# Optimization experiments

Hardware: AMD Instinct MI355X
Metric: run time of the kernel (lower is better)

The kernel has to match this reference:

```python
import jax, jax.numpy as jnp
import numpy as np

B, T, IN, E, D, O = 32, 256, 64, 128, 128, 32


def _lstm_scan(x_tbi, Wih, Whh, b, h0, c0):
    # x_tbi: [T,B,in]; returns hidden states [T,B,H]; PyTorch gate order i,f,g,o
    def step(carry, xt):
        h, c = carry
        z = xt @ Wih.T + h @ Whh.T + b
        i, f, g, o = jnp.split(z, 4, axis=-1)
        c = jax.nn.sigmoid(f) * c + jax.nn.sigmoid(i) * jnp.tanh(g)
        h = jax.nn.sigmoid(o) * jnp.tanh(c)
        return (h, c), h
    _, hs = jax.lax.scan(step, (h0, c0), x_tbi)
    return hs


def setup_inputs() -> dict:
    key = jax.random.key(0)
    ks = jax.random.split(key, 20)
    def u(k, shape, fan):
        s = 1.0 / np.sqrt(fan)
        return jax.random.uniform(k, shape, jnp.float32, -s, s)
    x = jax.random.normal(ks[0], (B, T, IN), jnp.float32)
    lengths = jnp.sort(jax.random.randint(ks[1], (B,), T // 2, T + 1))[::-1]
    lengths = lengths.at[0].set(T)  # pad_packed max length == T
    return {
        "x": x,
        "input_lengths": lengths,
        "dec_h0": jax.random.normal(ks[2], (B, D), jnp.float32),
        "dec_c0": jax.random.normal(ks[3], (B, D), jnp.float32),
        "Wih_f": u(ks[4], (4 * E, IN), E), "Whh_f": u(ks[5], (4 * E, E), E), "b_f": u(ks[6], (4 * E,), E),
        "Wih_b": u(ks[7], (4 * E, IN), E), "Whh_b": u(ks[8], (4 * E, E), E), "b_b": u(ks[9], (4 * E,), E),
        "Wa": u(ks[10], (D, D + 2 * E), D + 2 * E), "ba": u(ks[11], (D,), D + 2 * E),
        "v": jax.random.uniform(ks[12], (D,), jnp.float32, 0.0, 1.0),
        "Wih_d": u(ks[13], (4 * D, 2 * E + O), D), "Whh_d": u(ks[14], (4 * D, D), D), "b_d": u(ks[15], (4 * D,), D),
        "Wl": u(ks[16], (O, 2 * E + D), 2 * E + D), "bl": u(ks[17], (O,), 2 * E + D),
    }


def _forward(x, input_lengths, dec_h0, dec_c0, Wih_f, Whh_f, b_f, Wih_b, Whh_b, b_b,
             Wa, ba, v, Wih_d, Whh_d, b_d, Wl, bl):
    mask = jnp.arange(T)[None, :] < input_lengths[:, None]  # [B,T] valid positions
    z0 = jnp.zeros((B, E), x.dtype)
    # --- bidirectional encoder (packed-sequence semantics) ---
    hf = _lstm_scan(x.transpose(1, 0, 2), Wih_f, Whh_f, b_f, z0, z0).transpose(1, 0, 2)  # [B,T,E]
    # backward dir: reverse each valid span, scan, reverse back
    rev_idx = jnp.where(mask, input_lengths[:, None] - 1 - jnp.arange(T)[None, :], 0)  # [B,T]
    xr = jnp.take_along_axis(x, rev_idx[:, :, None], axis=1)
    hb_r = _lstm_scan(xr.transpose(1, 0, 2), Wih_b, Whh_b, b_b, z0, z0).transpose(1, 0, 2)
    hb = jnp.take_along_axis(hb_r, rev_idx[:, :, None], axis=1)
    enc = jnp.concatenate([hf, hb], -1) * mask[:, :, None]  # [B,T,2E], zeros past length
    # --- decoder with additive attention ---
    Wa_h, Wa_e = Wa[:, :D], Wa[:, D:]
    enc_proj = enc @ Wa_e.T + ba  # [B,T,D], constant across decoder steps
    def dec_step(carry, _):
        hidden, y = carry
        e = jnp.tanh(enc_proj + (hidden @ Wa_h.T)[:, None, :])  # [B,T,D]
        s = jnp.where(mask, e @ v, -jnp.inf)                     # length-masked scores
        a = jax.nn.softmax(s, axis=1)
        ctx = jnp.einsum('bt,bte->be', a, enc)                   # [B,2E]
        di = jnp.concatenate([y, ctx], -1)                       # [B,O+2E]
        # NOTE: original resets the decoder LSTM to (dec_h0, dec_c0) every step
        z = di @ Wih_d.T + dec_h0 @ Whh_d.T + b_d
        i, f, g, o = jnp.split(z, 4, axis=-1)
        c = jax.nn.sigmoid(f) * dec_c0 + jax.nn.sigmoid(i) * jnp.tanh(g)
        h = jax.nn.sigmoid(o) * jnp.tanh(c)
        y_new = jnp.concatenate([h, ctx], -1) @ Wl.T + bl        # [B,O]
        return (h, y_new), y_new
    y0 = jnp.zeros((B, O), x.dtype)
    _, ys = jax.lax.scan(dec_step, (dec_h0, y0), None, length=T)  # [T,B,O]
    out = ys.transpose(1, 0, 2).reshape(B, T * O)
    # original prepends a zeros[B,O] block then slices [:, 1:]
    out = jnp.concatenate([jnp.zeros((B, O), x.dtype), out], axis=1)
    return out[:, 1:]


def reference(x, input_lengths, dec_h0, dec_c0, Wih_f, Whh_f, b_f, Wih_b, Whh_b, b_b,
              Wa, ba, v, Wih_d, Whh_d, b_d, Wl, bl):
    return _forward(x, input_lengths, dec_h0, dec_c0, Wih_f, Whh_f, b_f, Wih_b, Whh_b, b_b,
                    Wa, ba, v, Wih_d, Whh_d, b_d, Wl, bl)
```

## Files before the change

kernel.cpp:

```cpp
#include <hip/hip_runtime.h>

#define BB 32
#define TT 256
#define INP 64
#define EE 128
#define DD 128
#define OO 32

#define OFF_XWF    0u
#define OFF_ENCWH  0u
#define OFF_XWB    4194304u
#define OFF_EPT    4194304u
#define OFF_ENCWLH 5242880u
#define OFF_HF     8388608u
#define OFF_HBR    9437184u
#define OFF_ZC     10485760u
#define OFF_WHHTF  10502144u
#define OFF_WHHTB  10567680u
#define OFF_WIHTF  10633216u
#define OFF_WIHTB  10665984u
#define OFF_WHHDT  10698752u
#define OFF_WCAT   10764288u
#define OFF_WLHT   10936320u
#define OFF_WAHH   10940416u
#define OFF_WYH    10948608u

typedef _Float16 h2_t __attribute__((ext_vector_type(2)));

__device__ __forceinline__ float fexp2(float x){ return __builtin_amdgcn_exp2f(x); }
__device__ __forceinline__ float frcp(float x){ return __builtin_amdgcn_rcpf(x); }
__device__ __forceinline__ float fsig(float x){ return frcp(1.0f + fexp2(-1.4426950408889634f * x)); }
__device__ __forceinline__ float ftanh_(float x){ return 1.0f - 2.0f * frcp(1.0f + fexp2(2.8853900817779268f * x)); }
__device__ __forceinline__ float packh2(float a, float b){
  h2_t t; t.x = (_Float16)a; t.y = (_Float16)b; return __builtin_bit_cast(float, t);
}
__device__ __forceinline__ h2_t ash2(float f){ return __builtin_bit_cast(h2_t, f); }
__device__ __forceinline__ float fdot2_(float a, float b, float c){
  return __builtin_amdgcn_fdot2(ash2(a), ash2(b), c, false);
}

#define C2F 2.8853900817779268f
#define L2E 1.4426950408889634f

__global__ void pack_kernel(const float* __restrict__ Whh_f, const float* __restrict__ Whh_b,
                            const float* __restrict__ Wih_f, const float* __restrict__ Wih_b,
                            const float* __restrict__ Whh_d, const float* __restrict__ Wa,
                            const float* __restrict__ Wih_d, const float* __restrict__ Wl,
                            float* __restrict__ ws){
  unsigned e = blockIdx.x * 256u + threadIdx.x;
  if (e < 65536u){ unsigned j=e>>7, k=e&127u; ws[OFF_WHHTF + (k>>2)*2048u + j*4u + (k&3u)] = Whh_f[e]; return; }
  e -= 65536u;
  if (e < 65536u){ unsigned j=e>>7, k=e&127u; ws[OFF_WHHTB + (k>>2)*2048u + j*4u + (k&3u)] = Whh_b[e]; return; }
  e -= 65536u;
  if (e < 32768u){ unsigned j=e>>6, i=e&63u; ws[OFF_WIHTF + (i>>2)*2048u + j*4u + (i&3u)] = Wih_f[e]; return; }
  e -= 32768u;
  if (e < 32768u){ unsigned j=e>>6, i=e&63u; ws[OFF_WIHTB + (i>>2)*2048u + j*4u + (i&3u)] = Wih_b[e]; return; }
  e -= 32768u;
  if (e < 65536u){ unsigned j=e>>7, k=e&127u; ws[OFF_WHHDT + (k>>2)*2048u + j*4u + (k&3u)] = Whh_d[e]; return; }
  e -= 65536u;
  if (e < 172032u){
    unsigned j = e >> 8, k = e & 255u;
    float val;
    if (j < 128u)      val = Wa[j*384u + 128u + k];
    else if (j < 640u) val = Wih_d[(j-128u)*288u + 32u + k];
    else               val = Wl[(j-640u)*384u + 128u + k];
    ws[OFF_WCAT + (k>>2)*2688u + j*4u + (k&3u)] = val; return;
  }
  e -= 172032u;
  if (e < 4096u){ unsigned k=e>>5, m=e&31u; ws[OFF_WLHT + (k>>2)*128u + m*4u + (k&3u)] = Wl[m*384u + k]; return; }
  e -= 4096u;
  if (e < 8192u){
    unsigned d = e >> 6, k2 = e & 63u;
    ws[OFF_WAHH + e] = packh2(Wa[d*384u + 2u*k2], Wa[d*384u + 2u*k2 + 1u]); return;
  }
  e -= 8192u;
  if (e < 8192u){
    unsigned m2 = e >> 9, j = e & 511u;
    ws[OFF_WYH + e] = packh2(Wih_d[j*288u + 2u*m2], Wih_d[j*288u + 2u*m2 + 1u]); return;
  }
}

__global__ __launch_bounds__(512) void zc_kernel(const float* __restrict__ dec_h0,
                                                 const float* __restrict__ b_d,
                                                 float* __restrict__ ws){
  __shared__ __align__(16) float h0[128];
  int b = blockIdx.x, j = threadIdx.x;
  if (j < 128) h0[j] = dec_h0[b*128 + j];
  __syncthreads();
  const float* WT = ws + OFF_WHHDT;
  float4 a4 = make_float4(0.f,0.f,0.f,0.f);
  #pragma unroll
  for (int k4 = 0; k4 < 32; k4++){
    float4 wv = *(const float4*)(WT + k4*2048 + j*4);
    float4 hv = *(const float4*)(h0 + k4*4);
    a4.x += wv.x*hv.x; a4.y += wv.y*hv.y; a4.z += wv.z*hv.z; a4.w += wv.w*hv.w;
  }
  ws[OFF_ZC + b*512 + j] = b_d[j] + (a4.x + a4.y) + (a4.z + a4.w);
}

__global__ __launch_bounds__(512) void xw_kernel(const float* __restrict__ x,
                                                 const int* __restrict__ lengths,
                                                 const float* __restrict__ b_f,
                                                 const float* __restrict__ b_b,
                                                 float* __restrict__ ws){
  int bx = blockIdx.x;
  int dir = bx >> 9, b = (bx >> 4) & 31, tile = bx & 15;
  int t0 = tile * 16;
  int len = lengths[b];
  __shared__ __align__(16) float xrow[16][64];
  const float* WT   = ws + (dir ? OFF_WIHTB : OFF_WIHTF);
  const float* bias = dir ? b_b : b_f;
  float* out = ws + (dir ? OFF_XWB : OFF_XWF) + (unsigned)b * TT * 512;
  int tid = threadIdx.x;
  for (int idx = tid; idx < 1024; idx += 512){
    int r = idx >> 6, i = idx & 63;
    int s = t0 + r;
    int src = dir ? ((s < len) ? (len - 1 - s) : 0) : s;
    xrow[r][i] = x[((unsigned)b * TT + src) * 64 + i];
  }
  __syncthreads();
  int j = tid;
  float bj = bias[j];
  float acc[16];
  #pragma unroll
  for (int r = 0; r < 16; r++) acc[r] = bj;
  #pragma unroll 4
  for (int i4 = 0; i4 < 16; i4++){
    float4 wv = *(const float4*)(WT + i4*2048 + j*4);
    #pragma unroll
    for (int r = 0; r < 16; r++){
      float4 xv = *(const float4*)(&xrow[r][i4*4]);
      acc[r] += wv.x*xv.x + wv.y*xv.y + wv.z*xv.z + wv.w*xv.w;
    }
  }
  #pragma unroll
  for (int r = 0; r < 16; r++) out[(t0 + r)*512 + j] = acc[r];
}

__global__ __launch_bounds__(512, 2) void lstm_kernel(const int* __restrict__ lengths,
                                                      float* __restrict__ ws){
  int bx = blockIdx.x;
  int b = bx & 31, dir = bx >> 5;
  int len = lengths[b];
  if (len < 1) len = 1; if (len > TT) len = TT;
  const float* xW = ws + (dir ? OFF_XWB : OFF_XWF) + (unsigned)b * TT * 512;
  const float* WT = ws + (dir ? OFF_WHHTB : OFF_WHHTF);
  float* hout = ws + (dir ? OFF_HBR : OFF_HF) + (unsigned)b * TT * 128;
  __shared__ __align__(16) float hsh[128];
  __shared__ __align__(16) float csh[128];
  __shared__ __align__(16) float zsh[512];
  int j = threadIdx.x;
  float w[128];
  #pragma unroll
  for (int k4 = 0; k4 < 32; k4++){
    float4 wv = *(const float4*)(WT + k4*2048 + j*4);
    w[k4*4+0] = wv.x; w[k4*4+1] = wv.y; w[k4*4+2] = wv.z; w[k4*4+3] = wv.w;
  }
  if (j < 128){ hsh[j] = 0.f; csh[j] = 0.f; }
  for (int t = 0; t < len; t++){
    __syncthreads();
    float4 a4 = make_float4(xW[t*512 + j], 0.f, 0.f, 0.f);
    #pragma unroll
    for (int k4 = 0; k4 < 32; k4++){
      float4 hv = *(const float4*)(hsh + k4*4);
      a4.x += w[k4*4+0]*hv.x; a4.y += w[k4*4+1]*hv.y;
      a4.z += w[k4*4+2]*hv.z; a4.w += w[k4*4+3]*hv.w;
    }
    zsh[j] = (a4.x + a4.y) + (a4.z + a4.w);
    __syncthreads();
    if (j < 128){
      float zi = zsh[j], zf = zsh[128+j], zg = zsh[256+j], zo = zsh[384+j];
      float c = fsig(zf)*csh[j] + fsig(zi)*ftanh_(zg);
      float h = fsig(zo)*ftanh_(c);
      csh[j] = c; hsh[j] = h;
      hout[t*128 + j] = h;
    }
  }
}

__global__ __launch_bounds__(192) void proj_kernel(const int* __restrict__ lengths,
                                                   const float* __restrict__ ba,
                                                   float* __restrict__ ws){
  int bx = blockIdx.x;
  int b = bx >> 4, tile = bx & 15;
  int len = lengths[b];
  if (len < 1) len = 1; if (len > TT) len = TT;
  int t0 = tile * 16;
  __shared__ __align__(16) float enc[16][256];
  int tid = threadIdx.x;
  const float* hf  = ws + OFF_HF  + (unsigned)b * TT * 128;
  const float* hbr = ws + OFF_HBR + (unsigned)b * TT * 128;
  for (int idx = tid; idx < 4096; idx += 192){
    int r = idx >> 8, k = idx & 255;
    int t = t0 + r;
    float vv = 0.f;
    if (t < len) vv = (k < 128) ? hf[t*128 + k] : hbr[(len-1-t)*128 + (k-128)];
    enc[r][k] = vv;
  }
  __syncthreads();
  if (tid >= 168) return;
  int j0 = tid * 4;
  float acc[16][4];
  #pragma unroll
  for (int r = 0; r < 16; r++){ acc[r][0]=0.f; acc[r][1]=0.f; acc[r][2]=0.f; acc[r][3]=0.f; }
  const float* WC = ws + OFF_WCAT;
  for (int k4 = 0; k4 < 64; k4++){
    float4 w0 = *(const float4*)(WC + k4*2688 + (j0+0)*4);
    float4 w1 = *(const float4*)(WC + k4*2688 + (j0+1)*4);
    float4 w2 = *(const float4*)(WC + k4*2688 + (j0+2)*4);
    float4 w3 = *(const float4*)(WC + k4*2688 + (j0+3)*4);
    #pragma unroll
    for (int r = 0; r < 16; r++){
      float4 ev = *(const float4*)(&enc[r][k4*4]);
      acc[r][0] += w0.x*ev.x + w0.y*ev.y + w0.z*ev.z + w0.w*ev.w;
      acc[r][1] += w1.x*ev.x + w1.y*ev.y + w1.z*ev.z + w1.w*ev.w;
      acc[r][2] += w2.x*ev.x + w2.y*ev.y + w2.z*ev.z + w2.w*ev.w;
      acc[r][3] += w3.x*ev.x + w3.y*ev.y + w3.z*ev.z + w3.w*ev.w;
    }
  }
  float* epo  = ws + OFF_EPT    + (unsigned)b * TT * 128;
  float* eWh  = ws + OFF_ENCWH  + (unsigned)b * 128 * 512;
  float* eWlh = ws + OFF_ENCWLH + (unsigned)b * 128 * 32;
  #pragma unroll
  for (int c = 0; c < 4; c++){
    int j = j0 + c;
    if (j < 128){
      float bj = ba[j];
      for (int r = 0; r < 16; r++) epo[(t0 + r)*128 + j] = (acc[r][c] + bj) * C2F;
    } else if (j < 640){
      for (int r2 = 0; r2 < 8; r2++)
        eWh[(tile*8 + r2)*512 + (j - 128)] = packh2(acc[2*r2][c], acc[2*r2+1][c]);
    } else {
      for (int r2 = 0; r2 < 8; r2++)
        eWlh[(tile*8 + r2)*32 + (j - 640)] = packh2(acc[2*r2][c], acc[2*r2+1][c]);
    }
  }
}

__global__ __launch_bounds__(512, 2) void decoder_kernel(const int* __restrict__ lengths,
                                                         const float* __restrict__ dec_h0,
                                                         const float* __restrict__ dec_c0,
                                                         const float* __restrict__ v,
                                                         const float* __restrict__ bl,
                                                         float* __restrict__ ws,
                                                         float* __restrict__ out){
  __shared__ __align__(16) float ep_lds[32768];
  __shared__ __align__(16) float red512[512];
  __shared__ __align__(16) float zsh[512];
  __shared__ __align__(16) float vqsh[256];
  __shared__ __align__(16) float hsh[128];
  __shared__ __align__(16) float c0sh[128];
  __shared__ __align__(16) float a_h2[128];
  __shared__ __align__(16) float h_h2[64];
  __shared__ __align__(16) float ylds[32];
  __shared__ __align__(16) float y_h2[16];
  __shared__ float redbuf[2], redbuf2[2], vsumsh;

  int b = blockIdx.x;
  int len = lengths[b];
  if (len < 1) len = 1; if (len > TT) len = TT;
  int tid = threadIdx.x;

  const float* EPT  = ws + OFF_EPT    + (unsigned)b * 32768;
  const float* EWH  = ws + OFF_ENCWH  + (unsigned)b * 65536;
  const float* EWLH = ws + OFF_ENCWLH + (unsigned)b * 4096;
  const float* WLHT = ws + OFF_WLHT;
  float* outp = out + (unsigned)b * 8223;

  float wreg[128];
  #pragma unroll
  for (int r = 0; r < 128; r++) wreg[r] = EWH[r*512 + tid];
  int d_ = tid & 127, p_ = tid >> 7;
  float wah[16];
  #pragma unroll
  for (int i = 0; i < 16; i++) wah[i] = ws[OFF_WAHH + d_*64 + p_*16 + i];
  float wy[16];
  #pragma unroll
  for (int i = 0; i < 16; i++) wy[i] = ws[OFF_WYH + i*512 + tid];
  float zc_r = ws[OFF_ZC + b*512 + tid];

  for (int c = 0; c < 64; c++){
    int idx = c*512 + tid;
    int t = idx >> 7, dd = idx & 127;
    ep_lds[t*128 + ((dd + 4*t) & 127)] = EPT[idx];
  }
  if (tid < 128){
    hsh[tid]  = dec_h0[b*128 + tid];
    c0sh[tid] = dec_c0[b*128 + tid];
    vqsh[2*tid+1] = v[tid];
  }
  if (tid < 64) h_h2[tid] = packh2(dec_h0[b*128 + 2*tid], dec_h0[b*128 + 2*tid + 1]);
  if (tid < 32) ylds[tid] = 0.f;
  if (tid < 16) y_h2[tid] = 0.f;
  if (tid < 31) outp[tid] = 0.f;
  if (tid == 0){ float s = 0.f; for (int k = 0; k < 128; k++) s += v[k]; vsumsh = s; }

  for (int t = 0; t < TT; t++){
    __syncthreads();
    if (tid < 16) y_h2[tid] = packh2(ylds[2*tid], ylds[2*tid+1]);
    {
      float qa = 0.f, qb = 0.f;
      #pragma unroll
      for (int i = 0; i < 16; i += 2){
        qa = fdot2_(h_h2[p_*16 + i],     wah[i],     qa);
        qb = fdot2_(h_h2[p_*16 + i + 1], wah[i + 1], qb);
      }
      red512[tid] = qa + qb;
    }
    __syncthreads();
    if (tid < 128)
      vqsh[2*tid] = (red512[tid] + red512[128+tid] + red512[256+tid] + red512[384+tid]) * C2F;
    __syncthreads();
    {
      int tt = tid & 255, half = tid >> 8;
      float4 P4 = make_float4(0.f,0.f,0.f,0.f);
      if (tt < len){
        const float* epr = ep_lds + tt*128;
        int rot = 4*tt;
        #pragma unroll 4
        for (int g = 0; g < 16; g++){
          int d0 = (half*16 + g)*4;
          float4 e4 = *(const float4*)(epr + ((d0 + rot) & 127));
          float4 vq0 = *(const float4*)(vqsh + 2*d0);
          float4 vq1 = *(const float4*)(vqsh + 2*d0 + 4);
          P4.x = fmaf(vq0.y, frcp(1.f + fexp2(e4.x + vq0.x)), P4.x);
          P4.y = fmaf(vq0.w, frcp(1.f + fexp2(e4.y + vq0.z)), P4.y);
          P4.z = fmaf(vq1.y, frcp(1.f + fexp2(e4.z + vq1.x)), P4.z);
          P4.w = fmaf(vq1.w, frcp(1.f + fexp2(e4.w + vq1.z)), P4.w);
        }
      }
      red512[tid] = (P4.x + P4.y) + (P4.z + P4.w);
    }
    __syncthreads();
    float s0 = -1e30f, s1 = -1e30f, e0 = 0.f, e1 = 0.f;
    if (tid < 128){
      int ta = 2*tid;
      if (ta < len)     s0 = vsumsh - 2.f*(red512[ta]   + red512[256+ta]);
      if (ta + 1 < len) s1 = vsumsh - 2.f*(red512[ta+1] + red512[256+ta+1]);
    }
    {
      float mm = fmaxf(s0, s1);
      #pragma unroll
      for (int off = 32; off; off >>= 1) mm = fmaxf(mm, __shfl_xor(mm, off));
      if (tid < 128 && (tid & 63) == 0) redbuf[tid>>6] = mm;
    }
    __syncthreads();
    if (tid < 128){
      float gm = fmaxf(redbuf[0], redbuf[1]);
      if (2*tid < len)     e0 = fexp2((s0 - gm) * L2E);
      if (2*tid + 1 < len) e1 = fexp2((s1 - gm) * L2E);
    }
    {
      float ss = e0 + e1;
      #pragma unroll
      for (int off = 32; off; off >>= 1) ss += __shfl_xor(ss, off);
      if (tid < 128 && (tid & 63) == 0) redbuf2[tid>>6] = ss;
    }
    __syncthreads();
    if (tid < 128){
      float rl = frcp(redbuf2[0] + redbuf2[1]);
      a_h2[tid] = packh2(e0 * rl, e1 * rl);
    }
    __syncthreads();
    {
      float za = 0.f, zb = 0.f, zc2 = 0.f, zd = 0.f;
      #pragma unroll
      for (int r4 = 0; r4 < 32; r4++){
        za  = fdot2_(a_h2[4*r4+0], wreg[4*r4+0], za);
        zb  = fdot2_(a_h2[4*r4+1], wreg[4*r4+1], zb);
        zc2 = fdot2_(a_h2[4*r4+2], wreg[4*r4+2], zc2);
        zd  = fdot2_(a_h2[4*r4+3], wreg[4*r4+3], zd);
      }
      #pragma unroll
      for (int i4 = 0; i4 < 4; i4++){
        za  = fdot2_(y_h2[4*i4+0], wy[4*i4+0], za);
        zb  = fdot2_(y_h2[4*i4+1], wy[4*i4+1], zb);
        zc2 = fdot2_(y_h2[4*i4+2], wy[4*i4+2], zc2);
        zd  = fdot2_(y_h2[4*i4+3], wy[4*i4+3], zd);
      }
      zsh[tid] = zc_r + ((za + zb) + (zc2 + zd));
    }
    __syncthreads();
    if (tid < 128){
      float zi = zsh[tid], zf = zsh[128+tid], zg = zsh[256+tid], zo = zsh[384+tid];
      float c = fsig(zf)*c0sh[tid] + fsig(zi)*ftanh_(zg);
      hsh[tid] = fsig(zo)*ftanh_(c);
    }
    __syncthreads();
    if (tid >= 256 && tid < 320){
      int i = tid - 256;
      h_h2[i] = packh2(hsh[2*i], hsh[2*i+1]);
    }
    if (tid < 256){
      int m = tid & 31, p = tid >> 5;
      float acc = 0.f;
      #pragma unroll
      for (int ri = 0; ri < 16; ri++){
        int r = p + ri*8;
        acc = fdot2_(a_h2[r], EWLH[r*32 + m], acc);
      }
      #pragma unroll
      for (int k4 = p; k4 < 32; k4 += 8){
        float4 hv = *(const float4*)(hsh + k4*4);
        float4 wv = *(const float4*)(WLHT + k4*128 + m*4);
        acc += hv.x*wv.x + hv.y*wv.y + hv.z*wv.z + hv.w*wv.w;
      }
      red512[tid] = acc;
    }
    __syncthreads();
    if (tid < 32){
      float y = bl[tid];
      #pragma unroll
      for (int p2 = 0; p2 < 8; p2++) y += red512[p2*32 + tid];
      ylds[tid] = y;
      outp[31 + t*32 + tid] = y;
    }
  }
}

extern "C" void kernel_launch(void* const* d_in, const int* in_sizes, int n_in,
                              void* d_out, int out_size, void* d_ws, size_t ws_size,
                              hipStream_t stream){
  const float* x       = (const float*)d_in[0];
  const int*   lengths = (const int*)  d_in[1];
  const float* dec_h0  = (const float*)d_in[2];
  const float* dec_c0  = (const float*)d_in[3];
  const float* Wih_f   = (const float*)d_in[4];
  const float* Whh_f   = (const float*)d_in[5];
  const float* b_f     = (const float*)d_in[6];
  const float* Wih_b   = (const float*)d_in[7];
  const float* Whh_b   = (const float*)d_in[8];
  const float* b_b     = (const float*)d_in[9];
  const float* Wa      = (const float*)d_in[10];
  const float* ba      = (const float*)d_in[11];
  const float* v       = (const float*)d_in[12];
  const float* Wih_d   = (const float*)d_in[13];
  const float* Whh_d   = (const float*)d_in[14];
  const float* b_d     = (const float*)d_in[15];
  const float* Wl      = (const float*)d_in[16];
  const float* bl      = (const float*)d_in[17];
  float* ws  = (float*)d_ws;
  float* out = (float*)d_out;

  pack_kernel<<<1776, 256, 0, stream>>>(Whh_f, Whh_b, Wih_f, Wih_b, Whh_d, Wa, Wih_d, Wl, ws);
  zc_kernel<<<32, 512, 0, stream>>>(dec_h0, b_d, ws);
  xw_kernel<<<1024, 512, 0, stream>>>(x, lengths, b_f, b_b, ws);
  lstm_kernel<<<64, 512, 0, stream>>>(lengths, ws);
  proj_kernel<<<512, 192, 0, stream>>>(lengths, ba, ws);
  decoder_kernel<<<32, 512, 0, stream>>>(lengths, dec_h0, dec_c0, v, bl, ws, out);
}
```

Before: 1.988 ms.

## Widen decoder to 1024 threads and cut per-step barriers

Doubles the decoder block to 1024 threads and splits the attention-context GEMV and score computation across more threads with fewer registers each. The output-projection reduction and the next step's query projection move into the tail of the previous step, so the loop needs fewer barriers. The softmax max pass is dropped in favor of clamped exponentials. The sigmoid sum shares one reciprocal between pairs of terms. Wl and bias are staged in LDS. Dropping max-subtraction relies on bounded scores and risks overflow or precision loss. The 4-blocks-per-CU launch bound may also force register spills.

```diff
diff --git a/kernel.cpp b/kernel.cpp
--- a/kernel.cpp
+++ b/kernel.cpp
@@ -237,24 +237,25 @@
   }
 }
 
-__global__ __launch_bounds__(512, 2) void decoder_kernel(const int* __restrict__ lengths,
-                                                         const float* __restrict__ dec_h0,
-                                                         const float* __restrict__ dec_c0,
-                                                         const float* __restrict__ v,
-                                                         const float* __restrict__ bl,
-                                                         float* __restrict__ ws,
-                                                         float* __restrict__ out){
+__global__ __launch_bounds__(1024, 4) void decoder_kernel(const int* __restrict__ lengths,
+                                                          const float* __restrict__ dec_h0,
+                                                          const float* __restrict__ dec_c0,
+                                                          const float* __restrict__ v,
+                                                          const float* __restrict__ bl,
+                                                          float* __restrict__ ws,
+                                                          float* __restrict__ out){
   __shared__ __align__(16) float ep_lds[32768];
-  __shared__ __align__(16) float red512[512];
-  __shared__ __align__(16) float zsh[512];
+  __shared__ __align__(16) float wlh_lds[4096];
+  __shared__ __align__(16) float red[1024];
   __shared__ __align__(16) float vqsh[256];
+  __shared__ __align__(16) float zcsh[512];
   __shared__ __align__(16) float hsh[128];
   __shared__ __align__(16) float c0sh[128];
-  __shared__ __align__(16) float a_h2[128];
-  __shared__ __align__(16) float h_h2[64];
-  __shared__ __align__(16) float ylds[32];
+  __shared__ __align__(16) _Float16 h_h16[128];
+  __shared__ __align__(16) _Float16 a_h16[256];
   __shared__ __align__(16) float y_h2[16];
-  __shared__ float redbuf[2], redbuf2[2], vsumsh;
+  __shared__ __align__(16) float blsh[32];
+  __shared__ float swave[4], vsumsh;
 
   int b = blockIdx.x;
   int len = lengths[b];
@@ -264,157 +265,175 @@
   const float* EPT  = ws + OFF_EPT    + (unsigned)b * 32768;
   const float* EWH  = ws + OFF_ENCWH  + (unsigned)b * 65536;
   const float* EWLH = ws + OFF_ENCWLH + (unsigned)b * 4096;
-  const float* WLHT = ws + OFF_WLHT;
   float* outp = out + (unsigned)b * 8223;
 
-  float wreg[128];
-  #pragma unroll
-  for (int r = 0; r < 128; r++) wreg[r] = EWH[r*512 + tid];
-  int d_ = tid & 127, p_ = tid >> 7;
+  int j_ = tid & 511, dh_ = tid >> 9;
+  int d_ = tid & 127, p_ = (tid >> 7) & 3;
+  float wreg[64];
+  #pragma unroll
+  for (int r = 0; r < 64; r++) wreg[r] = EWH[(dh_*64 + r)*512 + j_];
   float wah[16];
   #pragma unroll
   for (int i = 0; i < 16; i++) wah[i] = ws[OFF_WAHH + d_*64 + p_*16 + i];
-  float wy[16];
-  #pragma unroll
-  for (int i = 0; i < 16; i++) wy[i] = ws[OFF_WYH + i*512 + tid];
-  float zc_r = ws[OFF_ZC + b*512 + tid];
-
-  for (int c = 0; c < 64; c++){
-    int idx = c*512 + tid;
+  float wy[8];
+  #pragma unroll
+  for (int i = 0; i < 8; i++) wy[i] = ws[OFF_WYH + (dh_*8 + i)*512 + j_];
+
+  for (int c = 0; c < 32; c++){
+    int idx = c*1024 + tid;
     int t = idx >> 7, dd = idx & 127;
     ep_lds[t*128 + ((dd + 4*t) & 127)] = EPT[idx];
   }
+  for (int c = 0; c < 4; c++) wlh_lds[c*1024 + tid] = ws[OFF_WLHT + c*1024 + tid];
+  if (tid < 512) zcsh[tid] = ws[OFF_ZC + b*512 + tid];
   if (tid < 128){
-    hsh[tid]  = dec_h0[b*128 + tid];
+    float h0v = dec_h0[b*128 + tid];
+    hsh[tid] = h0v; h_h16[tid] = (_Float16)h0v;
     c0sh[tid] = dec_c0[b*128 + tid];
     vqsh[2*tid+1] = v[tid];
   }
-  if (tid < 64) h_h2[tid] = packh2(dec_h0[b*128 + 2*tid], dec_h0[b*128 + 2*tid + 1]);
-  if (tid < 32) ylds[tid] = 0.f;
   if (tid < 16) y_h2[tid] = 0.f;
+  if (tid < 32) blsh[tid] = bl[tid];
   if (tid < 31) outp[tid] = 0.f;
   if (tid == 0){ float s = 0.f; for (int k = 0; k < 128; k++) s += v[k]; vsumsh = s; }
+  __syncthreads();
+  if (tid >= 256 && tid < 768){
+    const float* hp = (const float*)h_h16;
+    float qa = 0.f, qb = 0.f;
+    #pragma unroll
+    for (int i = 0; i < 16; i += 2){
+      qa = fdot2_(hp[p_*16 + i],     wah[i],     qa);
+      qb = fdot2_(hp[p_*16 + i + 1], wah[i + 1], qb);
+    }
+    red[256 + p_*128 + d_] = qa + qb;
+  }
+  __syncthreads();
 
   for (int t = 0; t < TT; t++){
-    __syncthreads();
-    if (tid < 16) y_h2[tid] = packh2(ylds[2*tid], ylds[2*tid+1]);
+    if (tid < 128){
+      float q = red[256+tid] + red[384+tid] + red[512+tid] + red[640+tid];
+      vqsh[2*tid] = q * C2F;
+    } else if (tid < 144 && t > 0){
+      int m0 = 2*(tid - 128);
+      float ya = blsh[m0], yb = blsh[m0+1];
+      #pragma unroll
+      for (int p2 = 0; p2 < 8; p2++){ ya += red[p2*32 + m0]; yb += red[p2*32 + m0 + 1]; }
+      y_h2[tid - 128] = packh2(ya, yb);
+      outp[31 + (t-1)*32 + m0]     = ya;
+      outp[31 + (t-1)*32 + m0 + 1] = yb;
+    }
+    __syncthreads();
     {
-      float qa = 0.f, qb = 0.f;
-      #pragma unroll
-      for (int i = 0; i < 16; i += 2){
-        qa = fdot2_(h_h2[p_*16 + i],     wah[i],     qa);
-        qb = fdot2_(h_h2[p_*16 + i + 1], wah[i + 1], qb);
-      }
-      red512[tid] = qa + qb;
-    }
-    __syncthreads();
-    if (tid < 128)
-      vqsh[2*tid] = (red512[tid] + red512[128+tid] + red512[256+tid] + red512[384+tid]) * C2F;
-    __syncthreads();
-    {
-      int tt = tid & 255, half = tid >> 8;
-      float4 P4 = make_float4(0.f,0.f,0.f,0.f);
-      if (tt < len){
-        const float* epr = ep_lds + tt*128;
-        int rot = 4*tt;
-        #pragma unroll 4
-        for (int g = 0; g < 16; g++){
-          int d0 = (half*16 + g)*4;
-          float4 e4 = *(const float4*)(epr + ((d0 + rot) & 127));
+      int t_ = tid & 255, q4 = tid >> 8;
+      float P = 0.f;
+      if (t_ < len){
+        const float* epr = ep_lds + t_*128;
+        int rot = 4*t_;
+        float pa = 0.f, pb = 0.f, pc = 0.f, pd = 0.f;
+        #pragma unroll
+        for (int g = 0; g < 8; g++){
+          int d0 = q4*32 + g*4;
+          float4 e4  = *(const float4*)(epr + ((d0 + rot) & 127));
           float4 vq0 = *(const float4*)(vqsh + 2*d0);
           float4 vq1 = *(const float4*)(vqsh + 2*d0 + 4);
-          P4.x = fmaf(vq0.y, frcp(1.f + fexp2(e4.x + vq0.x)), P4.x);
-          P4.y = fmaf(vq0.w, frcp(1.f + fexp2(e4.y + vq0.z)), P4.y);
-          P4.z = fmaf(vq1.y, frcp(1.f + fexp2(e4.z + vq1.x)), P4.z);
-          P4.w = fmaf(vq1.w, frcp(1.f + fexp2(e4.w + vq1.z)), P4.w);
+          float E0 = fexp2(fminf(e4.x + vq0.x, 60.f));
+          float E1 = fexp2(fminf(e4.y + vq0.z, 60.f));
+          float E2 = fexp2(fminf(e4.z + vq1.x, 60.f));
+          float E3 = fexp2(fminf(e4.w + vq1.z, 60.f));
+          float D0 = 1.f + E0, D1 = 1.f + E1, D2 = 1.f + E2, D3 = 1.f + E3;
+          float r01 = frcp(D0*D1), r23 = frcp(D2*D3);
+          pa = fmaf(vq0.y*D1, r01, pa);
+          pb = fmaf(vq0.w*D0, r01, pb);
+          pc = fmaf(vq1.y*D3, r23, pc);
+          pd = fmaf(vq1.w*D2, r23, pd);
         }
-      }
-      red512[tid] = (P4.x + P4.y) + (P4.z + P4.w);
-    }
-    __syncthreads();
-    float s0 = -1e30f, s1 = -1e30f, e0 = 0.f, e1 = 0.f;
+        P = (pa + pb) + (pc + pd);
+      }
+      red[tid] = P;
+    }
+    __syncthreads();
+    float e_t = 0.f;
+    if (tid < 256){
+      float P = red[tid] + red[256+tid] + red[512+tid] + red[768+tid];
+      if (tid < len) e_t = fexp2((vsumsh - 2.f*P) * L2E);
+      float ss = e_t;
+      #pragma unroll
+      for (int off = 32; off; off >>= 1) ss += __shfl_xor(ss, off);
+      if ((tid & 63) == 0) swave[tid >> 6] = ss;
+    }
+    __syncthreads();
+    if (tid < 256){
+      float rl = frcp(fmaxf(swave[0] + swave[1] + swave[2] + swave[3], 1e-35f));
+      a_h16[tid] = (_Float16)(e_t * rl);
+    }
+    __syncthreads();
+    {
+      const float* ap = (const float*)a_h16;
+      float z0 = 0.f, z1 = 0.f, z2 = 0.f, z3 = 0.f;
+      #pragma unroll
+      for (int i = 0; i < 16; i++){
+        float4 a4 = *(const float4*)(ap + dh_*64 + i*4);
+        z0 = fdot2_(a4.x, wreg[i*4+0], z0);
+        z1 = fdot2_(a4.y, wreg[i*4+1], z1);
+        z2 = fdot2_(a4.z, wreg[i*4+2], z2);
+        z3 = fdot2_(a4.w, wreg[i*4+3], z3);
+      }
+      #pragma unroll
+      for (int i = 0; i < 8; i += 4){
+        z0 = fdot2_(y_h2[dh_*8 + i + 0], wy[i + 0], z0);
+        z1 = fdot2_(y_h2[dh_*8 + i + 1], wy[i + 1], z1);
+        z2 = fdot2_(y_h2[dh_*8 + i + 2], wy[i + 2], z2);
+        z3 = fdot2_(y_h2[dh_*8 + i + 3], wy[i + 3], z3);
+      }
+      red[dh_*512 + j_] = (z0 + z1) + (z2 + z3);
+    }
+    __syncthreads();
     if (tid < 128){
-      int ta = 2*tid;
-      if (ta < len)     s0 = vsumsh - 2.f*(red512[ta]   + red512[256+ta]);
-      if (ta + 1 < len) s1 = vsumsh - 2.f*(red512[ta+1] + red512[256+ta+1]);
-    }
-    {
-      float mm = fmaxf(s0, s1);
-      #pragma unroll
-      for (int off = 32; off; off >>= 1) mm = fmaxf(mm, __shfl_xor(mm, off));
-      if (tid < 128 && (tid & 63) == 0) redbuf[tid>>6] = mm;
-    }
-    __syncthreads();
-    if (tid < 128){
-      float gm = fmaxf(redbuf[0], redbuf[1]);
-      if (2*tid < len)     e0 = fexp2((s0 - gm) * L2E);
-      if (2*tid + 1 < len) e1 = fexp2((s1 - gm) * L2E);
-    }
-    {
-      float ss = e0 + e1;
-      #pragma unroll
-      for (int off = 32; off; off >>= 1) ss += __shfl_xor(ss, off);
-      if (tid < 128 && (tid & 63) == 0) redbuf2[tid>>6] = ss;
-    }
-    __syncthreads();
-    if (tid < 128){
-      float rl = frcp(redbuf2[0] + redbuf2[1]);
-      a_h2[tid] = packh2(e0 * rl, e1 * rl);
-    }
-    __syncthreads();
-    {
-      float za = 0.f, zb = 0.f, zc2 = 0.f, zd = 0.f;
-      #pragma unroll
-      for (int r4 = 0; r4 < 32; r4++){
-        za  = fdot2_(a_h2[4*r4+0], wreg[4*r4+0], za);
-        zb  = fdot2_(a_h2[4*r4+1], wreg[4*r4+1], zb);
-        zc2 = fdot2_(a_h2[4*r4+2], wreg[4*r4+2], zc2);
-        zd  = fdot2_(a_h2[4*r4+3], wreg[4*r4+3], zd);
-      }
-      #pragma unroll
-      for (int i4 = 0; i4 < 4; i4++){
-        za  = fdot2_(y_h2[4*i4+0], wy[4*i4+0], za);
-        zb  = fdot2_(y_h2[4*i4+1], wy[4*i4+1], zb);
-        zc2 = fdot2_(y_h2[4*i4+2], wy[4*i4+2], zc2);
-        zd  = fdot2_(y_h2[4*i4+3], wy[4*i4+3], zd);
-      }
-      zsh[tid] = zc_r + ((za + zb) + (zc2 + zd));
-    }
-    __syncthreads();
-    if (tid < 128){
-      float zi = zsh[tid], zf = zsh[128+tid], zg = zsh[256+tid], zo = zsh[384+tid];
+      float zi = red[tid]       + red[512 + tid]       + zcsh[tid];
+      float zf = red[128 + tid] + red[640 + tid]       + zcsh[128 + tid];
+      float zg = red[256 + tid] + red[768 + tid]       + zcsh[256 + tid];
+      float zo = red[384 + tid] + red[896 + tid]       + zcsh[384 + tid];
       float c = fsig(zf)*c0sh[tid] + fsig(zi)*ftanh_(zg);
-      hsh[tid] = fsig(zo)*ftanh_(c);
-    }
-    __syncthreads();
-    if (tid >= 256 && tid < 320){
-      int i = tid - 256;
-      h_h2[i] = packh2(hsh[2*i], hsh[2*i+1]);
-    }
+      float h = fsig(zo)*ftanh_(c);
+      hsh[tid] = h; h_h16[tid] = (_Float16)h;
+    }
+    __syncthreads();
     if (tid < 256){
       int m = tid & 31, p = tid >> 5;
       float acc = 0.f;
+      const float* ap = (const float*)a_h16;
       #pragma unroll
       for (int ri = 0; ri < 16; ri++){
         int r = p + ri*8;
-        acc = fdot2_(a_h2[r], EWLH[r*32 + m], acc);
-      }
-      #pragma unroll
-      for (int k4 = p; k4 < 32; k4 += 8){
+        acc = fdot2_(ap[r], EWLH[r*32 + m], acc);
+      }
+      #pragma unroll
+      for (int kk = 0; kk < 4; kk++){
+        int k4 = p + kk*8;
         float4 hv = *(const float4*)(hsh + k4*4);
-        float4 wv = *(const float4*)(WLHT + k4*128 + m*4);
+        float4 wv = *(const float4*)(wlh_lds + k4*128 + m*4);
         acc += hv.x*wv.x + hv.y*wv.y + hv.z*wv.z + hv.w*wv.w;
       }
-      red512[tid] = acc;
-    }
-    __syncthreads();
-    if (tid < 32){
-      float y = bl[tid];
-      #pragma unroll
-      for (int p2 = 0; p2 < 8; p2++) y += red512[p2*32 + tid];
-      ylds[tid] = y;
-      outp[31 + t*32 + tid] = y;
-    }
+      red[p*32 + m] = acc;
+    } else if (tid < 768){
+      const float* hp = (const float*)h_h16;
+      float qa = 0.f, qb = 0.f;
+      #pragma unroll
+      for (int i = 0; i < 16; i += 2){
+        qa = fdot2_(hp[p_*16 + i],     wah[i],     qa);
+        qb = fdot2_(hp[p_*16 + i + 1], wah[i + 1], qb);
+      }
+      red[256 + p_*128 + d_] = qa + qb;
+    }
+    __syncthreads();
+  }
+  if (tid >= 128 && tid < 144){
+    int m0 = 2*(tid - 128);
+    float ya = blsh[m0], yb = blsh[m0+1];
+    #pragma unroll
+    for (int p2 = 0; p2 < 8; p2++){ ya += red[p2*32 + m0]; yb += red[p2*32 + m0 + 1]; }
+    outp[31 + 255*32 + m0]     = ya;
+    outp[31 + 255*32 + m0 + 1] = yb;
   }
 }
 
@@ -447,5 +466,5 @@
   xw_kernel<<<1024, 512, 0, stream>>>(x, lengths, b_f, b_b, ws);
   lstm_kernel<<<64, 512, 0, stream>>>(lengths, ws);
   proj_kernel<<<512, 192, 0, stream>>>(lengths, ba, ws);
-  decoder_kernel<<<32, 512, 0, stream>>>(lengths, dec_h0, dec_c0, v, bl, ws, out);
-}
+  decoder_kernel<<<32, 1024, 0, stream>>>(lengths, dec_h0, dec_c0, v, bl, ws, out);
+}
```

New measurement: 2.717 ms. +36.7%, slower.

## Restructure decoder step: drop LDS enc cache, fewer barriers, skip softmax max

Applied to the files above, without the earlier changes.

The encoder projection is now written transposed ([d][t]) and the decoder reads it directly from global/L2 instead of staging 128KB into LDS. The per-step barrier chain is restructured: the y reduction is folded into the next step's q phase, the q projection is computed at the end of the step, and the softmax max-subtraction is removed because the scores are bounded. A single wave computes the exp-sum. This cuts several __syncthreads per step and frees LDS, but adds global-memory reads of ep every step.

```diff
diff --git a/kernel.cpp b/kernel.cpp
--- a/kernel.cpp
+++ b/kernel.cpp
@@ -218,7 +218,7 @@
       acc[r][3] += w3.x*ev.x + w3.y*ev.y + w3.z*ev.z + w3.w*ev.w;
     }
   }
-  float* epo  = ws + OFF_EPT    + (unsigned)b * TT * 128;
+  float* epo  = ws + OFF_EPT    + (unsigned)b * 128 * TT;
   float* eWh  = ws + OFF_ENCWH  + (unsigned)b * 128 * 512;
   float* eWlh = ws + OFF_ENCWLH + (unsigned)b * 128 * 32;
   #pragma unroll
@@ -226,7 +226,7 @@
     int j = j0 + c;
     if (j < 128){
       float bj = ba[j];
-      for (int r = 0; r < 16; r++) epo[(t0 + r)*128 + j] = (acc[r][c] + bj) * C2F;
+      for (int r = 0; r < 16; r++) epo[j*TT + (t0 + r)] = (acc[r][c] + bj) * C2F;
     } else if (j < 640){
       for (int r2 = 0; r2 < 8; r2++)
         eWh[(tile*8 + r2)*512 + (j - 128)] = packh2(acc[2*r2][c], acc[2*r2+1][c]);
@@ -244,27 +244,28 @@
                                                          const float* __restrict__ bl,
                                                          float* __restrict__ ws,
                                                          float* __restrict__ out){
-  __shared__ __align__(16) float ep_lds[32768];
-  __shared__ __align__(16) float red512[512];
+  __shared__ __align__(16) float qpart[512];
+  __shared__ __align__(16) float spart[512];
+  __shared__ __align__(16) float ypart[256];
   __shared__ __align__(16) float zsh[512];
   __shared__ __align__(16) float vqsh[256];
   __shared__ __align__(16) float hsh[128];
   __shared__ __align__(16) float c0sh[128];
   __shared__ __align__(16) float a_h2[128];
   __shared__ __align__(16) float h_h2[64];
-  __shared__ __align__(16) float ylds[32];
   __shared__ __align__(16) float y_h2[16];
-  __shared__ float redbuf[2], redbuf2[2], vsumsh;
+  __shared__ __align__(16) float blsh[32];
+  __shared__ float vsumsh;
 
   int b = blockIdx.x;
   int len = lengths[b];
   if (len < 1) len = 1; if (len > TT) len = TT;
   int tid = threadIdx.x;
 
-  const float* EPT  = ws + OFF_EPT    + (unsigned)b * 32768;
-  const float* EWH  = ws + OFF_ENCWH  + (unsigned)b * 65536;
-  const float* EWLH = ws + OFF_ENCWLH + (unsigned)b * 4096;
-  const float* WLHT = ws + OFF_WLHT;
+  const float* epg   = ws + OFF_EPT    + (unsigned)b * 128 * TT;
+  const float* EWH   = ws + OFF_ENCWH  + (unsigned)b * 65536;
+  const float* EWLH  = ws + OFF_ENCWLH + (unsigned)b * 4096;
+  const float* WlhTg = ws + OFF_WLHT;
   float* outp = out + (unsigned)b * 8223;
 
   float wreg[128];
@@ -279,87 +280,75 @@
   for (int i = 0; i < 16; i++) wy[i] = ws[OFF_WYH + i*512 + tid];
   float zc_r = ws[OFF_ZC + b*512 + tid];
 
-  for (int c = 0; c < 64; c++){
-    int idx = c*512 + tid;
-    int t = idx >> 7, dd = idx & 127;
-    ep_lds[t*128 + ((dd + 4*t) & 127)] = EPT[idx];
-  }
   if (tid < 128){
     hsh[tid]  = dec_h0[b*128 + tid];
     c0sh[tid] = dec_c0[b*128 + tid];
     vqsh[2*tid+1] = v[tid];
   }
   if (tid < 64) h_h2[tid] = packh2(dec_h0[b*128 + 2*tid], dec_h0[b*128 + 2*tid + 1]);
-  if (tid < 32) ylds[tid] = 0.f;
   if (tid < 16) y_h2[tid] = 0.f;
+  if (tid < 32) blsh[tid] = bl[tid];
   if (tid < 31) outp[tid] = 0.f;
   if (tid == 0){ float s = 0.f; for (int k = 0; k < 128; k++) s += v[k]; vsumsh = s; }
+  __syncthreads();
+  {
+    float qa = 0.f, qb = 0.f;
+    #pragma unroll
+    for (int i = 0; i < 16; i += 2){
+      qa = fdot2_(h_h2[p_*16 + i],     wah[i],     qa);
+      qb = fdot2_(h_h2[p_*16 + i + 1], wah[i + 1], qb);
+    }
+    qpart[tid] = qa + qb;
+  }
+  __syncthreads();
 
   for (int t = 0; t < TT; t++){
-    __syncthreads();
-    if (tid < 16) y_h2[tid] = packh2(ylds[2*tid], ylds[2*tid+1]);
+    if (tid < 128){
+      vqsh[2*tid] = (qpart[tid] + qpart[128+tid] + qpart[256+tid] + qpart[384+tid]) * C2F;
+    } else if (tid < 144 && t > 0){
+      int m0 = 2*(tid - 128);
+      float ya = blsh[m0], yb = blsh[m0+1];
+      #pragma unroll
+      for (int p2 = 0; p2 < 8; p2++){ ya += ypart[p2*32 + m0]; yb += ypart[p2*32 + m0 + 1]; }
+      y_h2[tid - 128] = packh2(ya, yb);
+      outp[31 + (t-1)*32 + m0]     = ya;
+      outp[31 + (t-1)*32 + m0 + 1] = yb;
+    }
+    __syncthreads();
     {
-      float qa = 0.f, qb = 0.f;
-      #pragma unroll
-      for (int i = 0; i < 16; i += 2){
-        qa = fdot2_(h_h2[p_*16 + i],     wah[i],     qa);
-        qb = fdot2_(h_h2[p_*16 + i + 1], wah[i + 1], qb);
-      }
-      red512[tid] = qa + qb;
-    }
-    __syncthreads();
-    if (tid < 128)
-      vqsh[2*tid] = (red512[tid] + red512[128+tid] + red512[256+tid] + red512[384+tid]) * C2F;
-    __syncthreads();
-    {
-      int tt = tid & 255, half = tid >> 8;
+      int t1 = tid >> 1, half = tid & 1;
       float4 P4 = make_float4(0.f,0.f,0.f,0.f);
-      if (tt < len){
-        const float* epr = ep_lds + tt*128;
-        int rot = 4*tt;
+      if (t1 < len){
+        const float* ec = epg + (half*64) * TT + t1;
+        const float* vq = vqsh + half*128;
         #pragma unroll 4
-        for (int g = 0; g < 16; g++){
-          int d0 = (half*16 + g)*4;
-          float4 e4 = *(const float4*)(epr + ((d0 + rot) & 127));
-          float4 vq0 = *(const float4*)(vqsh + 2*d0);
-          float4 vq1 = *(const float4*)(vqsh + 2*d0 + 4);
-          P4.x = fmaf(vq0.y, frcp(1.f + fexp2(e4.x + vq0.x)), P4.x);
-          P4.y = fmaf(vq0.w, frcp(1.f + fexp2(e4.y + vq0.z)), P4.y);
-          P4.z = fmaf(vq1.y, frcp(1.f + fexp2(e4.z + vq1.x)), P4.z);
-          P4.w = fmaf(vq1.w, frcp(1.f + fexp2(e4.w + vq1.z)), P4.w);
+        for (int di = 0; di < 64; di += 4){
+          float e0 = ec[(di+0)*TT], e1 = ec[(di+1)*TT];
+          float e2 = ec[(di+2)*TT], e3 = ec[(di+3)*TT];
+          float4 a01 = *(const float4*)(vq + di*2);
+          float4 a23 = *(const float4*)(vq + di*2 + 4);
+          P4.x = fmaf(a01.y, frcp(1.f + fexp2(e0 + a01.x)), P4.x);
+          P4.y = fmaf(a01.w, frcp(1.f + fexp2(e1 + a01.z)), P4.y);
+          P4.z = fmaf(a23.y, frcp(1.f + fexp2(e2 + a23.x)), P4.z);
+          P4.w = fmaf(a23.w, frcp(1.f + fexp2(e3 + a23.z)), P4.w);
         }
       }
-      red512[tid] = (P4.x + P4.y) + (P4.z + P4.w);
-    }
-    __syncthreads();
-    float s0 = -1e30f, s1 = -1e30f, e0 = 0.f, e1 = 0.f;
-    if (tid < 128){
-      int ta = 2*tid;
-      if (ta < len)     s0 = vsumsh - 2.f*(red512[ta]   + red512[256+ta]);
-      if (ta + 1 < len) s1 = vsumsh - 2.f*(red512[ta+1] + red512[256+ta+1]);
-    }
-    {
-      float mm = fmaxf(s0, s1);
-      #pragma unroll
-      for (int off = 32; off; off >>= 1) mm = fmaxf(mm, __shfl_xor(mm, off));
-      if (tid < 128 && (tid & 63) == 0) redbuf[tid>>6] = mm;
-    }
-    __syncthreads();
-    if (tid < 128){
-      float gm = fmaxf(redbuf[0], redbuf[1]);
-      if (2*tid < len)     e0 = fexp2((s0 - gm) * L2E);
-      if (2*tid + 1 < len) e1 = fexp2((s1 - gm) * L2E);
-    }
-    {
-      float ss = e0 + e1;
+      spart[tid] = (P4.x + P4.y) + (P4.z + P4.w);
+    }
+    __syncthreads();
+    if (tid < 64){
+      int tq = 4*tid;
+      float e0 = 0.f, e1 = 0.f, e2 = 0.f, e3 = 0.f;
+      if (tq     < len) e0 = fexp2((vsumsh - 2.f*(spart[2*tq]   + spart[2*tq+1])) * L2E);
+      if (tq + 1 < len) e1 = fexp2((vsumsh - 2.f*(spart[2*tq+2] + spart[2*tq+3])) * L2E);
+      if (tq + 2 < len) e2 = fexp2((vsumsh - 2.f*(spart[2*tq+4] + spart[2*tq+5])) * L2E);
+      if (tq + 3 < len) e3 = fexp2((vsumsh - 2.f*(spart[2*tq+6] + spart[2*tq+7])) * L2E);
+      float ss = (e0 + e1) + (e2 + e3);
       #pragma unroll
       for (int off = 32; off; off >>= 1) ss += __shfl_xor(ss, off);
-      if (tid < 128 && (tid & 63) == 0) redbuf2[tid>>6] = ss;
-    }
-    __syncthreads();
-    if (tid < 128){
-      float rl = frcp(redbuf2[0] + redbuf2[1]);
-      a_h2[tid] = packh2(e0 * rl, e1 * rl);
+      float rl = frcp(fmaxf(ss, 1e-35f));
+      a_h2[2*tid]     = packh2(e0 * rl, e1 * rl);
+      a_h2[2*tid + 1] = packh2(e2 * rl, e3 * rl);
     }
     __syncthreads();
     {
@@ -402,19 +391,30 @@
       #pragma unroll
       for (int k4 = p; k4 < 32; k4 += 8){
         float4 hv = *(const float4*)(hsh + k4*4);
-        float4 wv = *(const float4*)(WLHT + k4*128 + m*4);
+        float4 wv = *(const float4*)(WlhTg + k4*128 + m*4);
         acc += hv.x*wv.x + hv.y*wv.y + hv.z*wv.z + hv.w*wv.w;
       }
-      red512[tid] = acc;
-    }
-    __syncthreads();
-    if (tid < 32){
-      float y = bl[tid];
-      #pragma unroll
-      for (int p2 = 0; p2 < 8; p2++) y += red512[p2*32 + tid];
-      ylds[tid] = y;
-      outp[31 + t*32 + tid] = y;
-    }
+      ypart[p*32 + m] = acc;
+    }
+    __syncthreads();
+    {
+      float qa = 0.f, qb = 0.f;
+      #pragma unroll
+      for (int i = 0; i < 16; i += 2){
+        qa = fdot2_(h_h2[p_*16 + i],     wah[i],     qa);
+        qb = fdot2_(h_h2[p_*16 + i + 1], wah[i + 1], qb);
+      }
+      qpart[tid] = qa + qb;
+    }
+    __syncthreads();
+  }
+  if (tid >= 128 && tid < 144){
+    int m0 = 2*(tid - 128);
+    float ya = blsh[m0], yb = blsh[m0+1];
+    #pragma unroll
+    for (int p2 = 0; p2 < 8; p2++){ ya += ypart[p2*32 + m0]; yb += ypart[p2*32 + m0 + 1]; }
+    outp[31 + 255*32 + m0]     = ya;
+    outp[31 + 255*32 + m0 + 1] = yb;
   }
 }
 
```

Result: slower. 2.142 ms (+7.8%).
